# Performance work log

Measured on AMD Instinct MI355X. Metric: run time of the kernel, lower is better.

Reference implementation:

```python
import jax, jax.numpy as jnp
import numpy as np

N_NODES = 100000
N_EDGES = 1600000
HIDDEN = 128
N_LAYERS = 3
N_GRAPHS = 100
EPS = 1e-5


def setup_inputs() -> dict:
    key = jax.random.key(0)
    ks = jax.random.split(key, 9)
    node = jax.random.normal(ks[0], (N_NODES, HIDDEN), dtype=jnp.float32)
    edge_index = jax.random.randint(ks[1], (2, N_EDGES), 0, N_NODES, dtype=jnp.int32)
    edge_attr = jax.random.uniform(ks[2], (N_EDGES,), dtype=jnp.float32)
    batch_ptr = jnp.sort(jax.random.randint(ks[3], (N_NODES,), 0, N_GRAPHS, dtype=jnp.int32))
    W = jax.random.normal(ks[4], (N_LAYERS, HIDDEN, HIDDEN), dtype=jnp.float32) * (1.0 / np.sqrt(HIDDEN))
    b = jax.random.normal(ks[5], (N_LAYERS, HIDDEN), dtype=jnp.float32) * 0.02
    gn_weight = jnp.ones((N_LAYERS, HIDDEN), dtype=jnp.float32)
    gn_bias = jnp.zeros((N_LAYERS, HIDDEN), dtype=jnp.float32)
    gn_alpha = jnp.ones((N_LAYERS, HIDDEN), dtype=jnp.float32)
    return {"node": node, "edge_index": edge_index, "edge_attr": edge_attr,
            "batch_ptr": batch_ptr, "W": W, "b": b, "gn_weight": gn_weight,
            "gn_bias": gn_bias, "gn_alpha": gn_alpha}


def reference(node, edge_index, edge_attr, batch_ptr, W, b, gn_weight, gn_bias, gn_alpha):
    N, d = node.shape
    src, dst = edge_index[0], edge_index[1]
    # GCN normalization with self-loops (weight 1), as in PyG gcn_norm
    loop = jnp.arange(N, dtype=src.dtype)
    src_a = jnp.concatenate([src, loop])
    dst_a = jnp.concatenate([dst, loop])
    w_a = jnp.concatenate([edge_attr, jnp.ones((N,), dtype=edge_attr.dtype)])
    deg = jax.ops.segment_sum(w_a, dst_a, num_segments=N)
    dis = jnp.where(deg > 0, deg ** -0.5, 0.0)
    norm = dis[src_a] * w_a * dis[dst_a]  # [E+N]

    counts = jax.ops.segment_sum(jnp.ones((N,), node.dtype), batch_ptr,
                                 num_segments=N_GRAPHS)[:, None]  # [G,1]

    for l in range(W.shape[0]):
        # GCNConv: linear transform, then gather-normalize-scatter over edges
        h = node @ W[l]  # [N,d]
        agg = jax.ops.segment_sum(norm[:, None] * h[src_a], dst_a, num_segments=N) + b[l]
        # GraphNorm: per-graph mean shift (scaled by alpha) and variance norm
        mean = jax.ops.segment_sum(agg, batch_ptr, num_segments=N_GRAPHS) / counts  # [G,d]
        sub = agg - gn_alpha[l] * mean[batch_ptr]
        var = jax.ops.segment_sum(sub * sub, batch_ptr, num_segments=N_GRAPHS) / counts
        node = jax.nn.relu(gn_weight[l] * sub * jax.lax.rsqrt(var[batch_ptr] + EPS) + gn_bias[l])
    return node
```

## Files before the change

kernel.cpp:

```cpp
#include <hip/hip_runtime.h>
#include <cstdint>

#define N_N 100000
#define N_E 1600000
#define HID 128
#define N_G 100
#define EPSF 1e-5f

#define NB   256
#define EPB  ((N_E + NB - 1) / NB)
#define NBKT ((N_N + 255) >> 8)

#define MAXCH (N_N / 16 + N_G)

static inline int ceil_div(int a, int b){ return (a + b - 1) / b; }

typedef __attribute__((ext_vector_type(8))) short bf16x8;
typedef __attribute__((ext_vector_type(4))) float f32x4;

__device__ inline unsigned short f2bf(float f){
  unsigned int u = __float_as_uint(f);
  unsigned int r = u + 0x7fffu + ((u >> 16) & 1u);
  return (unsigned short)(r >> 16);
}
__device__ inline void fma8(float* acc, float nv, uint4 u){
  acc[0] += nv * __uint_as_float(u.x << 16);
  acc[1] += nv * __uint_as_float(u.x & 0xffff0000u);
  acc[2] += nv * __uint_as_float(u.y << 16);
  acc[3] += nv * __uint_as_float(u.y & 0xffff0000u);
  acc[4] += nv * __uint_as_float(u.z << 16);
  acc[5] += nv * __uint_as_float(u.z & 0xffff0000u);
  acc[6] += nv * __uint_as_float(u.w << 16);
  acc[7] += nv * __uint_as_float(u.w & 0xffff0000u);
}

__global__ void k_wt3(const float* __restrict__ W, unsigned short* __restrict__ Wt,
                      int* __restrict__ gstart, int* __restrict__ gend){
  int i = blockIdx.x * 256 + threadIdx.x;
  if (i < N_G){ gstart[i] = 0; gend[i] = 0; }
  if (i >= 3 * HID * HID) return;
  int l = i >> 14;
  int r = i & 16383;
  int n = r >> 7, k = r & 127;
  Wt[i] = f2bf(W[l * HID * HID + k * HID + n]);
}

__global__ void k_bnd(const int* __restrict__ bp, int* __restrict__ gstart,
                      int* __restrict__ gend){
  int i = blockIdx.x * 256 + threadIdx.x;
  if (i >= N_N) return;
  int g = bp[i];
  if (i == 0 || bp[i - 1] != g) gstart[g] = i;
  if (i == N_N - 1 || bp[i + 1] != g) gend[g] = i + 1;
}

__global__ void k_cbase(const int* __restrict__ gstart, const int* __restrict__ gend,
                        int* __restrict__ cbase){
  if (threadIdx.x == 0){
    int run = 0;
    for (int g = 0; g < N_G; ++g){
      cbase[g] = run;
      int len = gend[g] - gstart[g];
      run += (len + 15) >> 4;
    }
    cbase[N_G] = run;
  }
}

__global__ __launch_bounds__(256) void k_hist(const int* __restrict__ dst,
                                              int* __restrict__ counts){
  __shared__ int h[NBKT];
  int t = threadIdx.x, blk = blockIdx.x;
  for (int i = t; i < NBKT; i += 256) h[i] = 0;
  __syncthreads();
  int e0 = blk * EPB, e1 = min(e0 + EPB, N_E);
  for (int e = e0 + t; e < e1; e += 256)
    atomicAdd(&h[dst[e] >> 8], 1);
  __syncthreads();
  for (int i = t; i < NBKT; i += 256) counts[i * NB + blk] = h[i];
}

__global__ __launch_bounds__(256) void k_scanA(int* __restrict__ data,
                                               int* __restrict__ bsum, int n){
  __shared__ int s[256];
  int t = threadIdx.x;
  int i = blockIdx.x * 256 + t;
  int v = (i < n) ? data[i] : 0;
  s[t] = v; __syncthreads();
  #pragma unroll
  for (int off = 1; off < 256; off <<= 1){
    int tmp = (t >= off) ? s[t - off] : 0;
    __syncthreads();
    s[t] += tmp;
    __syncthreads();
  }
  if (i < n) data[i] = s[t] - v;
  if (t == 255) bsum[blockIdx.x] = s[255];
}

__global__ __launch_bounds__(512) void k_scanB(int* __restrict__ bsum, int nblocks){
  __shared__ int s[512];
  int t = threadIdx.x;
  int v = (t < nblocks) ? bsum[t] : 0;
  s[t] = v; __syncthreads();
  #pragma unroll
  for (int off = 1; off < 512; off <<= 1){
    int tmp = (t >= off) ? s[t - off] : 0;
    __syncthreads();
    s[t] += tmp;
    __syncthreads();
  }
  if (t < nblocks) bsum[t] = s[t] - v;
}

__global__ __launch_bounds__(256) void k_part(const int* __restrict__ src,
                                              const int* __restrict__ dst,
                                              const float* __restrict__ w,
                                              const int* __restrict__ coff,
                                              const int* __restrict__ bsum,
                                              int2* __restrict__ part){
  __shared__ int off[NBKT];
  int t = threadIdx.x, blk = blockIdx.x;
  for (int i = t; i < NBKT; i += 256)
    off[i] = coff[i * NB + blk] + bsum[i];
  __syncthreads();
  int e0 = blk * EPB, e1 = min(e0 + EPB, N_E);
  for (int e = e0 + t; e < e1; e += 256){
    int d = dst[e];
    int pos = atomicAdd(&off[d >> 8], 1);
    part[pos] = make_int2(src[e] | ((d & 255) << 24), __float_as_int(w[e]));
  }
}

__global__ __launch_bounds__(256) void k_csr(const int* __restrict__ coff,
                                             const int* __restrict__ bsum,
                                             const int2* __restrict__ part,
                                             int2* __restrict__ edge8,
                                             int* __restrict__ ptr,
                                             float* __restrict__ dis,
                                             float* __restrict__ nself){
  __shared__ int h[256];
  __shared__ int c[256];
  __shared__ float wsum[256];
  __shared__ int s[256];
  int t = threadIdx.x, b = blockIdx.x;
  int base  = coff[b * NB] + bsum[b];
  int base2 = (b + 1 < NBKT) ? coff[(b + 1) * NB] + bsum[b + 1] : N_E;
  h[t] = 0; c[t] = 0; wsum[t] = 0.f;
  __syncthreads();
  for (int e = base + t; e < base2; e += 256){
    int2 v = part[e];
    int local = ((unsigned int)v.x) >> 24;
    atomicAdd(&h[local], 1);
    atomicAdd(&wsum[local], __int_as_float(v.y));
  }
  __syncthreads();
  int v0 = h[t];
  s[t] = v0; __syncthreads();
  #pragma unroll
  for (int off = 1; off < 256; off <<= 1){
    int tmp = (t >= off) ? s[t - off] : 0;
    __syncthreads();
    s[t] += tmp;
    __syncthreads();
  }
  int mybase = base + s[t] - v0;
  int node = (b << 8) + t;
  float dv = rsqrtf(1.0f + wsum[t]);
  if (node < N_N){
    ptr[node] = mybase;
    dis[node] = dv;
    nself[node] = dv * dv;
  }
  if (b == NBKT - 1 && t == 0) ptr[N_N] = N_E;
  h[t] = mybase;
  __syncthreads();
  wsum[t] = dv;
  __syncthreads();
  for (int e = base + t; e < base2; e += 256){
    int2 v = part[e];
    int local = ((unsigned int)v.x) >> 24;
    int pos = h[local] + atomicAdd(&c[local], 1);
    edge8[pos] = make_int2(v.x & 0x00ffffff,
                           __float_as_int(__int_as_float(v.y) * wsum[local]));
  }
}

__global__ void k_ne(const float* __restrict__ dis, int2* __restrict__ edge8){
  int e = blockIdx.x * 256 + threadIdx.x;
  if (e >= N_E) return;
  int2 v = edge8[e];
  v.y = __float_as_int(__int_as_float(v.y) * dis[v.x]);
  edge8[e] = v;
}

__global__ __launch_bounds__(256) void k_gemm(const float* __restrict__ X,
                                              const float* __restrict__ agg,
                                              int fused,
                                              const int* __restrict__ bp,
                                              const float* __restrict__ mean,
                                              const float* __restrict__ rstd,
                                              const float* __restrict__ alpha,
                                              const float* __restrict__ gwv,
                                              const float* __restrict__ gbv,
                                              const unsigned short* __restrict__ Wt,
                                              unsigned short* __restrict__ Hb, int nrows){
  __shared__ unsigned short lA[64 * 136];
  __shared__ unsigned short lB[128 * 136];
  int tid = threadIdx.x;
  int row0 = blockIdx.x * 64;

  #pragma unroll
  for (int i = 0; i < 8; ++i){
    int c = tid + i * 256;
    int r = c >> 4, cc = c & 15;
    *(uint4*)&lB[r * 136 + cc * 8] = ((const uint4*)Wt)[c];
  }
  #pragma unroll
  for (int i = 0; i < 8; ++i){
    int c = tid + i * 256;
    int r = c >> 5, cc = c & 31;
    int gr = row0 + r;
    float4 v = make_float4(0.f, 0.f, 0.f, 0.f);
    if (gr < nrows){
      if (!fused){
        v = *(const float4*)(X + (size_t)gr * HID + cc * 4);
      } else {
        int g = bp[gr];
        float4 a  = *(const float4*)(agg  + (size_t)gr * HID + cc * 4);
        float4 m  = *(const float4*)(mean + g * HID + cc * 4);
        float4 rs = *(const float4*)(rstd + g * HID + cc * 4);
        float4 al = *(const float4*)(alpha + cc * 4);
        float4 wv = *(const float4*)(gwv + cc * 4);
        float4 bv = *(const float4*)(gbv + cc * 4);
        v.x = fmaxf(wv.x * (a.x - al.x * m.x) * rs.x + bv.x, 0.f);
        v.y = fmaxf(wv.y * (a.y - al.y * m.y) * rs.y + bv.y, 0.f);
        v.z = fmaxf(wv.z * (a.z - al.z * m.z) * rs.z + bv.z, 0.f);
        v.w = fmaxf(wv.w * (a.w - al.w * m.w) * rs.w + bv.w, 0.f);
      }
    }
    unsigned short pk[4] = {f2bf(v.x), f2bf(v.y), f2bf(v.z), f2bf(v.w)};
    *(uint2*)&lA[r * 136 + cc * 4] = *(const uint2*)pk;
  }
  __syncthreads();

  int wave = tid >> 6;
  int lane = tid & 63;
  int l16 = lane & 15;
  int quad = lane >> 4;
  int am = wave * 16 + l16;

  bf16x8 afr[4];
  #pragma unroll
  for (int kc = 0; kc < 4; ++kc)
    afr[kc] = *(const bf16x8*)&lA[am * 136 + kc * 32 + quad * 8];

  f32x4 accs[8];
  #pragma unroll
  for (int nt = 0; nt < 8; ++nt){
    f32x4 acc = {0.f, 0.f, 0.f, 0.f};
    int bn = nt * 16 + l16;
    #pragma unroll
    for (int kc = 0; kc < 4; ++kc){
      bf16x8 bfr = *(const bf16x8*)&lB[bn * 136 + kc * 32 + quad * 8];
      acc = __builtin_amdgcn_mfma_f32_16x16x32_bf16(afr[kc], bfr, acc, 0, 0, 0);
    }
    accs[nt] = acc;
  }

  __syncthreads();
  int crow = wave * 16 + quad * 4;
  #pragma unroll
  for (int nt = 0; nt < 8; ++nt){
    int col = nt * 16 + l16;
    #pragma unroll
    for (int r = 0; r < 4; ++r)
      lA[(crow + r) * 136 + col] = f2bf(accs[nt][r]);
  }
  __syncthreads();
  #pragma unroll
  for (int i = 0; i < 4; ++i){
    int idx = i * 256 + tid;
    int row = idx >> 4, c8 = idx & 15;
    int gr = row0 + row;
    if (gr < nrows)
      *(uint4*)&Hb[(size_t)gr * HID + c8 * 8] = *(const uint4*)&lA[row * 136 + c8 * 8];
  }
}

__global__ __launch_bounds__(256) void k_gather(const int* __restrict__ ptr,
                                                const int2* __restrict__ edge8,
                                                const unsigned short* __restrict__ Hb,
                                                const float* __restrict__ nself,
                                                const float* __restrict__ bias,
                                                float* __restrict__ agg,
                                                const int* __restrict__ cbase,
                                                const int* __restrict__ gstart,
                                                const int* __restrict__ gend,
                                                float* __restrict__ psum,
                                                float* __restrict__ psq){
  __shared__ float rs[16][132];
  __shared__ float rq[16][132];
  int blk = blockIdx.x;
  if (blk >= cbase[N_G]) return;
  int lo = 0, hi = N_G;
  while (hi - lo > 1){ int mid = (lo + hi) >> 1; if (cbase[mid] <= blk) lo = mid; else hi = mid; }
  int g = lo;
  int row0 = gstart[g] + (blk - cbase[g]) * 16;
  int rend = gend[g];
  int trow = threadIdx.x >> 4;
  int lane = threadIdx.x & 15;
  int node = row0 + trow;
  bool active = node < rend;
  const uint4* h16 = (const uint4*)Hb;
  float4 b0 = ((const float4*)bias)[lane * 2];
  float4 b1 = ((const float4*)bias)[lane * 2 + 1];
  float acc[8] = {b0.x, b0.y, b0.z, b0.w, b1.x, b1.y, b1.z, b1.w};
  if (active){
    float ns = nself[node];
    uint4 hu = h16[(size_t)node * 16 + lane];
    fma8(acc, ns, hu);
    int e0 = ptr[node], e1 = ptr[node + 1];
    int e = e0;
    for (; e + 4 <= e1; e += 4){
      int2 ev0 = edge8[e + 0];
      int2 ev1 = edge8[e + 1];
      int2 ev2 = edge8[e + 2];
      int2 ev3 = edge8[e + 3];
      uint4 r0 = h16[(size_t)ev0.x * 16 + lane];
      uint4 r1 = h16[(size_t)ev1.x * 16 + lane];
      uint4 r2 = h16[(size_t)ev2.x * 16 + lane];
      uint4 r3 = h16[(size_t)ev3.x * 16 + lane];
      fma8(acc, __int_as_float(ev0.y), r0);
      fma8(acc, __int_as_float(ev1.y), r1);
      fma8(acc, __int_as_float(ev2.y), r2);
      fma8(acc, __int_as_float(ev3.y), r3);
    }
    for (; e < e1; ++e){
      int2 ev = edge8[e];
      uint4 r0 = h16[(size_t)ev.x * 16 + lane];
      fma8(acc, __int_as_float(ev.y), r0);
    }
    float4* ap = (float4*)(agg + (size_t)node * HID + lane * 8);
    ap[0] = make_float4(acc[0], acc[1], acc[2], acc[3]);
    ap[1] = make_float4(acc[4], acc[5], acc[6], acc[7]);
  }
  int f = lane * 8;
  #pragma unroll
  for (int j = 0; j < 8; ++j){
    float v = active ? acc[j] : 0.f;
    rs[trow][f + j] = v;
    rq[trow][f + j] = v * v;
  }
  __syncthreads();
  if (threadIdx.x < 128){
    float s = 0.f, q = 0.f;
    #pragma unroll
    for (int r = 0; r < 16; ++r){ s += rs[r][threadIdx.x]; q += rq[r][threadIdx.x]; }
    psum[(size_t)blk * HID + threadIdx.x] = s;
    psq [(size_t)blk * HID + threadIdx.x] = q;
  }
}

__global__ void k_finstat(const float* __restrict__ psum, const float* __restrict__ psq,
                          const int* __restrict__ cbase,
                          const int* __restrict__ gstart, const int* __restrict__ gend,
                          const float* __restrict__ alpha,
                          float* __restrict__ mean, float* __restrict__ rstd){
  int i = blockIdx.x * 256 + threadIdx.x;
  if (i >= N_G * HID) return;
  int g = i >> 7, f = i & (HID - 1);
  int c0 = cbase[g], c1 = cbase[g + 1];
  float c = (float)(gend[g] - gstart[g]);
  float inv = c > 0.f ? 1.0f / c : 0.f;
  float sm = 0.f, sq = 0.f;
  for (int k = c0; k < c1; ++k){
    sm += psum[(size_t)k * HID + f];
    sq += psq [(size_t)k * HID + f];
  }
  float m = sm * inv;
  float ex2 = sq * inv;
  float al = alpha[f];
  float var = ex2 - m * m * al * (2.0f - al);
  mean[i] = m;
  rstd[i] = rsqrtf(var + EPSF);
}

__global__ void k_out(const float* __restrict__ agg, const int* __restrict__ bp,
                      const float* __restrict__ mean, const float* __restrict__ rstd,
                      const float* __restrict__ alpha, const float* __restrict__ gw,
                      const float* __restrict__ gb, float* __restrict__ out){
  int idx = blockIdx.x * 256 + threadIdx.x;
  if (idx >= N_N * 32) return;
  int i = idx >> 5, q = idx & 31;
  int g = bp[i];
  float4 a  = ((const float4*)agg)[idx];
  float4 m  = ((const float4*)mean)[g * 32 + q];
  float4 r  = ((const float4*)rstd)[g * 32 + q];
  float4 al = ((const float4*)alpha)[q];
  float4 wv = ((const float4*)gw)[q];
  float4 bv = ((const float4*)gb)[q];
  float4 o;
  o.x = fmaxf(wv.x * (a.x - al.x * m.x) * r.x + bv.x, 0.f);
  o.y = fmaxf(wv.y * (a.y - al.y * m.y) * r.y + bv.y, 0.f);
  o.z = fmaxf(wv.z * (a.z - al.z * m.z) * r.z + bv.z, 0.f);
  o.w = fmaxf(wv.w * (a.w - al.w * m.w) * r.w + bv.w, 0.f);
  ((float4*)out)[idx] = o;
}


extern "C" void kernel_launch(void* const* d_in, const int* in_sizes, int n_in,
                              void* d_out, int out_size, void* d_ws, size_t ws_size,
                              hipStream_t stream){
  const float* node0 = (const float*)d_in[0];
  const int*   eidx  = (const int*)d_in[1];
  const float* eattr = (const float*)d_in[2];
  const int*   bp    = (const int*)d_in[3];
  const float* W     = (const float*)d_in[4];
  const float* bias  = (const float*)d_in[5];
  const float* gw    = (const float*)d_in[6];
  const float* gb    = (const float*)d_in[7];
  const float* ga    = (const float*)d_in[8];
  float* out = (float*)d_out;
  const int* src = eidx;
  const int* dst = eidx + N_E;

  char* p = (char*)d_ws;
  auto carve = [&](size_t nbytes) -> char* {
    char* q = p; p += (nbytes + 255) & ~(size_t)255; return q;
  };
  float* dis    = (float*)carve((size_t)N_N * 4);
  float* nself  = (float*)carve((size_t)N_N * 4);
  int*   gstart = (int*)  carve((size_t)N_G * 4);
  int*   gend   = (int*)  carve((size_t)N_G * 4);
  int*   cbase  = (int*)  carve((size_t)(N_G + 1) * 4);
  int*   coff   = (int*)  carve((size_t)NBKT * NB * 4);
  int*   bsum   = (int*)  carve((size_t)512 * 4);
  int*   ptr    = (int*)  carve((size_t)(N_N + 1) * 4);
  int2*  edge8  = (int2*) carve((size_t)N_E * 8);
  unsigned short* hb = (unsigned short*)carve((size_t)N_N * HID * 2);
  unsigned short* wt = (unsigned short*)carve((size_t)3 * HID * HID * 2);
  float* agg    = (float*)carve((size_t)N_N * HID * 4);
  float* mean   = (float*)carve((size_t)N_G * HID * 4);
  float* rstd   = (float*)carve((size_t)N_G * HID * 4);
  float* psum   = (float*)carve((size_t)MAXCH * HID * 4);
  float* psq    = (float*)carve((size_t)MAXCH * HID * 4);
  int2*  part   = (int2*)agg;

  int nscan = NBKT * NB;
  int nscan_blocks = ceil_div(nscan, 256);

  k_wt3  <<<ceil_div(3 * HID * HID, 256), 256, 0, stream>>>(W, wt, gstart, gend);
  k_bnd  <<<ceil_div(N_N, 256), 256, 0, stream>>>(bp, gstart, gend);
  k_cbase<<<1, 64, 0, stream>>>(gstart, gend, cbase);
  k_hist <<<NB, 256, 0, stream>>>(dst, coff);
  k_scanA<<<nscan_blocks, 256, 0, stream>>>(coff, bsum, nscan);
  k_scanB<<<1, 512, 0, stream>>>(bsum, nscan_blocks);
  k_part <<<NB, 256, 0, stream>>>(src, dst, eattr, coff, bsum, part);
  k_csr  <<<NBKT, 256, 0, stream>>>(coff, bsum, part, edge8, ptr, dis, nself);
  k_ne   <<<ceil_div(N_E, 256), 256, 0, stream>>>(dis, edge8);

  for (int l = 0; l < 3; ++l){
    if (l == 0){
      k_gemm <<<ceil_div(N_N, 64), 256, 0, stream>>>(node0, nullptr, 0,
                 nullptr, nullptr, nullptr, nullptr, nullptr, nullptr,
                 wt, hb, N_N);
    } else {
      k_gemm <<<ceil_div(N_N, 64), 256, 0, stream>>>(nullptr, agg, 1,
                 bp, mean, rstd, ga + (l - 1) * HID, gw + (l - 1) * HID,
                 gb + (l - 1) * HID, wt + (size_t)l * HID * HID, hb, N_N);
    }
    k_gather <<<MAXCH, 256, 0, stream>>>(ptr, edge8, hb, nself,
                 bias + l * HID, agg, cbase, gstart, gend, psum, psq);
    k_finstat<<<ceil_div(N_G * HID, 256), 256, 0, stream>>>(psum, psq, cbase,
                 gstart, gend, ga + l * HID, mean, rstd);
  }
  k_out <<<ceil_div(N_N * 32, 256), 256, 0, stream>>>(agg, bp, mean, rstd,
             ga + 2 * HID, gw + 2 * HID, gb + 2 * HID, out);
}
```

Measured before the change: 574.6 us.

## Fold source-side degree scaling into GEMM epilogue and merge preprocessing kernels

```diff
diff --git a/kernel.cpp b/kernel.cpp
--- a/kernel.cpp
+++ b/kernel.cpp
@@ -10,6 +10,8 @@
 #define NB   256
 #define EPB  ((N_E + NB - 1) / NB)
 #define NBKT ((N_N + 255) >> 8)
+#define NBB  ((N_N + 255) / 256)
+#define NWT  ((3 * HID * HID) / 256)
 
 #define MAXCH (N_N / 16 + N_G)
 
@@ -34,50 +36,48 @@
   acc[7] += nv * __uint_as_float(u.w & 0xffff0000u);
 }
 
-__global__ void k_wt3(const float* __restrict__ W, unsigned short* __restrict__ Wt,
-                      int* __restrict__ gstart, int* __restrict__ gend){
-  int i = blockIdx.x * 256 + threadIdx.x;
-  if (i < N_G){ gstart[i] = 0; gend[i] = 0; }
-  if (i >= 3 * HID * HID) return;
-  int l = i >> 14;
-  int r = i & 16383;
-  int n = r >> 7, k = r & 127;
-  Wt[i] = f2bf(W[l * HID * HID + k * HID + n]);
-}
-
-__global__ void k_bnd(const int* __restrict__ bp, int* __restrict__ gstart,
-                      int* __restrict__ gend){
-  int i = blockIdx.x * 256 + threadIdx.x;
-  if (i >= N_N) return;
-  int g = bp[i];
-  if (i == 0 || bp[i - 1] != g) gstart[g] = i;
-  if (i == N_N - 1 || bp[i + 1] != g) gend[g] = i + 1;
-}
-
-__global__ void k_cbase(const int* __restrict__ gstart, const int* __restrict__ gend,
-                        int* __restrict__ cbase){
-  if (threadIdx.x == 0){
-    int run = 0;
-    for (int g = 0; g < N_G; ++g){
-      cbase[g] = run;
-      int len = gend[g] - gstart[g];
-      run += (len + 15) >> 4;
-    }
-    cbase[N_G] = run;
-  }
-}
-
-__global__ __launch_bounds__(256) void k_hist(const int* __restrict__ dst,
-                                              int* __restrict__ counts){
-  __shared__ int h[NBKT];
+__global__ __launch_bounds__(256) void k_pre(const int* __restrict__ dst,
+                                             int* __restrict__ counts,
+                                             const int* __restrict__ bp,
+                                             int* __restrict__ gstart,
+                                             int* __restrict__ gend,
+                                             const float* __restrict__ W,
+                                             unsigned short* __restrict__ Wt){
   int t = threadIdx.x, blk = blockIdx.x;
-  for (int i = t; i < NBKT; i += 256) h[i] = 0;
-  __syncthreads();
-  int e0 = blk * EPB, e1 = min(e0 + EPB, N_E);
-  for (int e = e0 + t; e < e1; e += 256)
-    atomicAdd(&h[dst[e] >> 8], 1);
-  __syncthreads();
-  for (int i = t; i < NBKT; i += 256) counts[i * NB + blk] = h[i];
+  if (blk < NB){
+    __shared__ int h[NBKT];
+    for (int i = t; i < NBKT; i += 256) h[i] = 0;
+    __syncthreads();
+    int e0 = blk * EPB, e1 = min(e0 + EPB, N_E);
+    for (int e = e0 + t; e < e1; e += 256)
+      atomicAdd(&h[dst[e] >> 8], 1);
+    __syncthreads();
+    for (int i = t; i < NBKT; i += 256) counts[i * NB + blk] = h[i];
+  } else if (blk < NB + NBB){
+    int i = (blk - NB) * 256 + t;
+    if (i >= N_N) return;
+    int g = bp[i];
+    if (i == 0){
+      gstart[g] = 0;
+      for (int gg = 0; gg < g; ++gg){ gstart[gg] = 0; gend[gg] = 0; }
+    } else {
+      int pg = bp[i - 1];
+      if (pg != g){
+        gend[pg] = i; gstart[g] = i;
+        for (int gg = pg + 1; gg < g; ++gg){ gstart[gg] = i; gend[gg] = i; }
+      }
+    }
+    if (i == N_N - 1){
+      gend[g] = N_N;
+      for (int gg = g + 1; gg < N_G; ++gg){ gstart[gg] = N_N; gend[gg] = N_N; }
+    }
+  } else {
+    int j = (blk - NB - NBB) * 256 + t;
+    int l = j >> 14;
+    int r = j & 16383;
+    int n = r >> 7, k = r & 127;
+    Wt[j] = f2bf(W[l * HID * HID + k * HID + n]);
+  }
 }
 
 __global__ __launch_bounds__(256) void k_scanA(int* __restrict__ data,
@@ -98,8 +98,12 @@
   if (t == 255) bsum[blockIdx.x] = s[255];
 }
 
-__global__ __launch_bounds__(512) void k_scanB(int* __restrict__ bsum, int nblocks){
+__global__ __launch_bounds__(512) void k_scanB(int* __restrict__ bsum, int nblocks,
+                                               const int* __restrict__ gstart,
+                                               const int* __restrict__ gend,
+                                               int* __restrict__ cbase){
   __shared__ int s[512];
+  __shared__ int cs[128];
   int t = threadIdx.x;
   int v = (t < nblocks) ? bsum[t] : 0;
   s[t] = v; __syncthreads();
@@ -111,6 +115,21 @@
     __syncthreads();
   }
   if (t < nblocks) bsum[t] = s[t] - v;
+  int cv = 0;
+  if (t < 128){
+    if (t < N_G) cv = (gend[t] - gstart[t] + 15) >> 4;
+    cs[t] = cv;
+  }
+  __syncthreads();
+  #pragma unroll
+  for (int off = 1; off < 128; off <<= 1){
+    int tmp = (t >= off && t < 128) ? cs[t - off] : 0;
+    __syncthreads();
+    if (t < 128) cs[t] += tmp;
+    __syncthreads();
+  }
+  if (t < N_G) cbase[t] = cs[t] - cv;
+  if (t == N_G - 1) cbase[N_G] = cs[t];
 }
 
 __global__ __launch_bounds__(256) void k_part(const int* __restrict__ src,
@@ -137,8 +156,7 @@
                                              const int2* __restrict__ part,
                                              int2* __restrict__ edge8,
                                              int* __restrict__ ptr,
-                                             float* __restrict__ dis,
-                                             float* __restrict__ nself){
+                                             float* __restrict__ dis){
   __shared__ int h[256];
   __shared__ int c[256];
   __shared__ float wsum[256];
@@ -170,7 +188,6 @@
   if (node < N_N){
     ptr[node] = mybase;
     dis[node] = dv;
-    nself[node] = dv * dv;
   }
   if (b == NBKT - 1 && t == 0) ptr[N_N] = N_E;
   h[t] = mybase;
@@ -184,14 +201,6 @@
     edge8[pos] = make_int2(v.x & 0x00ffffff,
                            __float_as_int(__int_as_float(v.y) * wsum[local]));
   }
-}
-
-__global__ void k_ne(const float* __restrict__ dis, int2* __restrict__ edge8){
-  int e = blockIdx.x * 256 + threadIdx.x;
-  if (e >= N_E) return;
-  int2 v = edge8[e];
-  v.y = __float_as_int(__int_as_float(v.y) * dis[v.x]);
-  edge8[e] = v;
 }
 
 __global__ __launch_bounds__(256) void k_gemm(const float* __restrict__ X,
@@ -204,6 +213,7 @@
                                               const float* __restrict__ gwv,
                                               const float* __restrict__ gbv,
                                               const unsigned short* __restrict__ Wt,
+                                              const float* __restrict__ dis,
                                               unsigned short* __restrict__ Hb, int nrows){
   __shared__ unsigned short lA[64 * 136];
   __shared__ unsigned short lB[128 * 136];
@@ -268,14 +278,21 @@
     accs[nt] = acc;
   }
 
-  __syncthreads();
   int crow = wave * 16 + quad * 4;
+  float ds[4];
+  #pragma unroll
+  for (int r = 0; r < 4; ++r){
+    int grr = row0 + crow + r;
+    ds[r] = (grr < nrows) ? dis[grr] : 0.f;
+  }
+
+  __syncthreads();
   #pragma unroll
   for (int nt = 0; nt < 8; ++nt){
     int col = nt * 16 + l16;
     #pragma unroll
     for (int r = 0; r < 4; ++r)
-      lA[(crow + r) * 136 + col] = f2bf(accs[nt][r]);
+      lA[(crow + r) * 136 + col] = f2bf(accs[nt][r] * ds[r]);
   }
   __syncthreads();
   #pragma unroll
@@ -291,7 +308,7 @@
 __global__ __launch_bounds__(256) void k_gather(const int* __restrict__ ptr,
                                                 const int2* __restrict__ edge8,
                                                 const unsigned short* __restrict__ Hb,
-                                                const float* __restrict__ nself,
+                                                const float* __restrict__ dis,
                                                 const float* __restrict__ bias,
                                                 float* __restrict__ agg,
                                                 const int* __restrict__ cbase,
@@ -299,8 +316,8 @@
                                                 const int* __restrict__ gend,
                                                 float* __restrict__ psum,
                                                 float* __restrict__ psq){
-  __shared__ float rs[16][132];
-  __shared__ float rq[16][132];
+  __shared__ float ws[4][128];
+  __shared__ float wq[4][128];
   int blk = blockIdx.x;
   if (blk >= cbase[N_G]) return;
   int lo = 0, hi = N_G;
@@ -317,7 +334,7 @@
   float4 b1 = ((const float4*)bias)[lane * 2 + 1];
   float acc[8] = {b0.x, b0.y, b0.z, b0.w, b1.x, b1.y, b1.z, b1.w};
   if (active){
-    float ns = nself[node];
+    float ns = dis[node];
     uint4 hu = h16[(size_t)node * 16 + lane];
     fma8(acc, ns, hu);
     int e0 = ptr[node], e1 = ptr[node + 1];
@@ -345,20 +362,23 @@
     ap[0] = make_float4(acc[0], acc[1], acc[2], acc[3]);
     ap[1] = make_float4(acc[4], acc[5], acc[6], acc[7]);
   }
-  int f = lane * 8;
+  int wv = threadIdx.x >> 6;
+  int liw = threadIdx.x & 63;
   #pragma unroll
   for (int j = 0; j < 8; ++j){
     float v = active ? acc[j] : 0.f;
-    rs[trow][f + j] = v;
-    rq[trow][f + j] = v * v;
+    float q = v * v;
+    v += __shfl_xor(v, 16); v += __shfl_xor(v, 32);
+    q += __shfl_xor(q, 16); q += __shfl_xor(q, 32);
+    if (liw < 16){ ws[wv][lane * 8 + j] = v; wq[wv][lane * 8 + j] = q; }
   }
   __syncthreads();
   if (threadIdx.x < 128){
-    float s = 0.f, q = 0.f;
-    #pragma unroll
-    for (int r = 0; r < 16; ++r){ s += rs[r][threadIdx.x]; q += rq[r][threadIdx.x]; }
-    psum[(size_t)blk * HID + threadIdx.x] = s;
-    psq [(size_t)blk * HID + threadIdx.x] = q;
+    int t = threadIdx.x;
+    float s = ws[0][t] + ws[1][t] + ws[2][t] + ws[3][t];
+    float q = wq[0][t] + wq[1][t] + wq[2][t] + wq[3][t];
+    psum[(size_t)blk * HID + t] = s;
+    psq [(size_t)blk * HID + t] = q;
   }
 }
 
@@ -430,7 +450,6 @@
     char* q = p; p += (nbytes + 255) & ~(size_t)255; return q;
   };
   float* dis    = (float*)carve((size_t)N_N * 4);
-  float* nself  = (float*)carve((size_t)N_N * 4);
   int*   gstart = (int*)  carve((size_t)N_G * 4);
   int*   gend   = (int*)  carve((size_t)N_G * 4);
   int*   cbase  = (int*)  carve((size_t)(N_G + 1) * 4);
@@ -450,27 +469,23 @@
   int nscan = NBKT * NB;
   int nscan_blocks = ceil_div(nscan, 256);
 
-  k_wt3  <<<ceil_div(3 * HID * HID, 256), 256, 0, stream>>>(W, wt, gstart, gend);
-  k_bnd  <<<ceil_div(N_N, 256), 256, 0, stream>>>(bp, gstart, gend);
-  k_cbase<<<1, 64, 0, stream>>>(gstart, gend, cbase);
-  k_hist <<<NB, 256, 0, stream>>>(dst, coff);
+  k_pre  <<<NB + NBB + NWT, 256, 0, stream>>>(dst, coff, bp, gstart, gend, W, wt);
   k_scanA<<<nscan_blocks, 256, 0, stream>>>(coff, bsum, nscan);
-  k_scanB<<<1, 512, 0, stream>>>(bsum, nscan_blocks);
+  k_scanB<<<1, 512, 0, stream>>>(bsum, nscan_blocks, gstart, gend, cbase);
   k_part <<<NB, 256, 0, stream>>>(src, dst, eattr, coff, bsum, part);
-  k_csr  <<<NBKT, 256, 0, stream>>>(coff, bsum, part, edge8, ptr, dis, nself);
-  k_ne   <<<ceil_div(N_E, 256), 256, 0, stream>>>(dis, edge8);
+  k_csr  <<<NBKT, 256, 0, stream>>>(coff, bsum, part, edge8, ptr, dis);
 
   for (int l = 0; l < 3; ++l){
     if (l == 0){
       k_gemm <<<ceil_div(N_N, 64), 256, 0, stream>>>(node0, nullptr, 0,
                  nullptr, nullptr, nullptr, nullptr, nullptr, nullptr,
-                 wt, hb, N_N);
+                 wt, dis, hb, N_N);
     } else {
       k_gemm <<<ceil_div(N_N, 64), 256, 0, stream>>>(nullptr, agg, 1,
                  bp, mean, rstd, ga + (l - 1) * HID, gw + (l - 1) * HID,
-                 gb + (l - 1) * HID, wt + (size_t)l * HID * HID, hb, N_N);
-    }
-    k_gather <<<MAXCH, 256, 0, stream>>>(ptr, edge8, hb, nself,
+                 gb + (l - 1) * HID, wt + (size_t)l * HID * HID, dis, hb, N_N);
+    }
+    k_gather <<<MAXCH, 256, 0, stream>>>(ptr, edge8, hb, dis,
                  bias + l * HID, agg, cbase, gstart, gend, psum, psq);
     k_finstat<<<ceil_div(N_G * HID, 256), 256, 0, stream>>>(psum, psq, cbase,
                  gstart, gend, ga + l * HID, mean, rstd);
```

Result: faster. 562.9 us (-2.0%).
